# Kernel optimization log

Measured on AMD Instinct MI355X. Metric: run time of the kernel, lower is better.

## Reference

```python
import jax, jax.numpy as jnp
import numpy as np

GRID_SIZE = 8
IN_DIM = 1024
OUT_DIM = 1024
BATCH = 4096


def setup_inputs() -> dict:
    key = jax.random.key(0)
    k1, k2, k3 = jax.random.split(key, 3)
    noise_scale = 0.1
    noise_scale_base = 0.1
    x = jax.random.normal(k1, (BATCH, IN_DIM), dtype=jnp.float32)
    scale_base = (1.0 / np.sqrt(IN_DIM)
                  + (jax.random.normal(k2, (OUT_DIM, IN_DIM), dtype=jnp.float32) * 2 - 1)
                  * noise_scale_base)
    scale_spline = jnp.full((OUT_DIM, IN_DIM), 1.0, dtype=jnp.float32)
    coeff = (jax.random.uniform(k3, (2, OUT_DIM, IN_DIM, GRID_SIZE), dtype=jnp.float32)
             * noise_scale / (np.sqrt(IN_DIM) * np.sqrt(GRID_SIZE)))
    return {"x": x, "scale_base": scale_base, "scale_spline": scale_spline,
            "coeff": coeff}


def reference(x, scale_base, scale_spline, coeff):
    # x: (B, I); scale_base/scale_spline: (O, I); coeff: (2, O, I, G)
    G = coeff.shape[-1]
    k = jnp.arange(1, G + 1, dtype=x.dtype)          # (G,)
    ang = x[:, :, None] * k                           # (B, I, G)
    cos_b = jnp.cos(ang)
    sin_b = jnp.sin(ang)
    # fold scale_spline into coeff: (2, O, I, G)
    w = scale_spline[None, :, :, None] * coeff
    spline = (jnp.einsum('big,oig->bo', cos_b, w[0])
              + jnp.einsum('big,oig->bo', sin_b, w[1]))  # (B, O)
    base = jnp.einsum('bi,oi->bo', jax.nn.silu(x), scale_base)
    return base + spline
```

## Files before the change

### kernel.cpp

```cpp
#include <hip/hip_runtime.h>
#include <hip/hip_bf16.h>
#include <stdint.h>

#define BATCH   4096
#define IN_DIM  1024
#define OUT_DIM 1024
#define GRID_G  8
#define K8      16384
#define KB      1024
#define SPLIT8  4
#define WSCALE  256.0f

typedef __bf16 bf16x8 __attribute__((ext_vector_type(8)));
typedef float  f32x4  __attribute__((ext_vector_type(4)));
typedef int    i32x4  __attribute__((ext_vector_type(4)));
typedef int    i32x8  __attribute__((ext_vector_type(8)));

__device__ inline void store_fp8x8(void* p, const float v[8]) {
    int lo = 0, hi = 0;
    lo = __builtin_amdgcn_cvt_pk_fp8_f32(v[0], v[1], lo, false);
    lo = __builtin_amdgcn_cvt_pk_fp8_f32(v[2], v[3], lo, true);
    hi = __builtin_amdgcn_cvt_pk_fp8_f32(v[4], v[5], hi, false);
    hi = __builtin_amdgcn_cvt_pk_fp8_f32(v[6], v[7], hi, true);
    *(int2*)p = make_int2(lo, hi);
}

__global__ void prep(const float* __restrict__ x, const float* __restrict__ sb,
                     const float* __restrict__ ss, const float* __restrict__ coeff,
                     uint8_t* __restrict__ A8, uint8_t* __restrict__ W8,
                     __bf16* __restrict__ Ab, __bf16* __restrict__ Wb) {
    if (blockIdx.x < 2048) {
        int t  = blockIdx.x * blockDim.x + threadIdx.x;
        int b  = t >> 7;
        int i0 = (t & 127) * 8;
        const float4* xp = (const float4*)(x + (size_t)b * IN_DIM + i0);
        float4 x0 = xp[0], x1 = xp[1];
        float xv[8] = {x0.x, x0.y, x0.z, x0.w, x1.x, x1.y, x1.z, x1.w};

        constexpr float INV2PI = 0.15915494309189535f;
        float c1[8], s1[8], ck[8], sk[8];
        bf16x8 v;
#pragma unroll
        for (int j = 0; j < 8; ++j) {
            float xx  = xv[j];
            float sil = xx / (1.f + __expf(-xx));
            v[j] = (__bf16)sil;
            float rev = xx * INV2PI;
            rev -= floorf(rev);
            s1[j] = __builtin_amdgcn_sinf(rev);
            c1[j] = __builtin_amdgcn_cosf(rev);
            ck[j] = c1[j]; sk[j] = s1[j];
        }
        *(bf16x8*)(Ab + (size_t)b * IN_DIM + i0) = v;

        uint8_t* a8 = A8 + (size_t)b * K8 + i0;
#pragma unroll
        for (int g = 1; g <= GRID_G; ++g) {
            float vc[8], vs[8];
#pragma unroll
            for (int j = 0; j < 8; ++j) {
                vc[j] = ck[j];
                vs[j] = sk[j];
                float cn = ck[j] * c1[j] - sk[j] * s1[j];
                float sn = sk[j] * c1[j] + ck[j] * s1[j];
                ck[j] = cn; sk[j] = sn;
            }
            store_fp8x8(a8 + (size_t)(g - 1) * IN_DIM, vc);
            store_fp8x8(a8 + (size_t)(GRID_G + g - 1) * IN_DIM, vs);
        }
    } else {
        int t  = (blockIdx.x - 2048) * blockDim.x + threadIdx.x;
        int o  = t >> 7;
        int i0 = (t & 127) * 8;
        size_t oi = (size_t)o * IN_DIM + i0;

        float s[8];
        {
            const float4* sp = (const float4*)(ss + oi);
            float4 s0 = sp[0], s1v = sp[1];
            s[0]=s0.x; s[1]=s0.y; s[2]=s0.z; s[3]=s0.w;
            s[4]=s1v.x; s[5]=s1v.y; s[6]=s1v.z; s[7]=s1v.w;
        }
        {
            const float4* bp = (const float4*)(sb + oi);
            float4 b0 = bp[0], b1 = bp[1];
            float bv[8] = {b0.x, b0.y, b0.z, b0.w, b1.x, b1.y, b1.z, b1.w};
            bf16x8 v;
#pragma unroll
            for (int j = 0; j < 8; ++j) v[j] = (__bf16)bv[j];
            *(bf16x8*)(Wb + oi) = v;
        }
        uint8_t* w8 = W8 + (size_t)o * K8 + i0;
#pragma unroll
        for (int p = 0; p < 2; ++p) {
            const float* cp = coeff + ((size_t)p * OUT_DIM * IN_DIM + oi) * GRID_G;
            float c[8][8];
#pragma unroll
            for (int j = 0; j < 8; ++j) {
                const float4* cj = (const float4*)(cp + (size_t)j * GRID_G);
                float4 a0 = cj[0], a1 = cj[1];
                c[j][0]=a0.x; c[j][1]=a0.y; c[j][2]=a0.z; c[j][3]=a0.w;
                c[j][4]=a1.x; c[j][5]=a1.y; c[j][6]=a1.z; c[j][7]=a1.w;
            }
#pragma unroll
            for (int g = 0; g < GRID_G; ++g) {
                float v[8];
#pragma unroll
                for (int j = 0; j < 8; ++j) v[j] = s[j] * c[j][g] * WSCALE;
                store_fp8x8(w8 + (size_t)(p * GRID_G + g) * IN_DIM, v);
            }
        }
    }
}

__global__ __launch_bounds__(256, 4) void gemm_all(const uint8_t* __restrict__ A8,
                                                   const uint8_t* __restrict__ W8,
                                                   const uint8_t* __restrict__ Ab,
                                                   const uint8_t* __restrict__ Wb,
                                                   float* __restrict__ C) {
    __shared__ __align__(16) uint8_t As[16384];
    __shared__ __align__(16) uint8_t Bs[16384];
    const int tid = threadIdx.x;
    const int w   = tid >> 6;
    const int l   = tid & 63;
    const int bn  = blockIdx.x;
    const int bm  = blockIdx.y;
    const int kz  = blockIdx.z;
    const int wm  = w & 1;
    const int wn  = w >> 1;

    f32x4 acc[4][4] = {};

    const int srow   = l >> 3;
    const int schunk = ((l & 7) ^ srow) * 16;
    const int lm = l & 15;
    const int q  = l >> 4;
    float oscale;

    if (kz < SPLIT8) {
        const uint8_t* Ag = A8 + (size_t)(bm * 128 + w * 32 + srow) * K8 + kz * (K8 / SPLIT8) + schunk;
        const uint8_t* Bg = W8 + (size_t)(bn * 128 + w * 32 + srow) * K8 + kz * (K8 / SPLIT8) + schunk;
        const int c0 = (q * 2) << 4, c1 = (q * 2 + 1) << 4;

        for (int ks = 0; ks < (K8 / SPLIT8) / 128; ++ks) {
#pragma unroll
            for (int j = 0; j < 4; ++j) {
                __builtin_amdgcn_global_load_lds(
                    (const uint32_t*)(Ag + (size_t)(j * 8) * K8),
                    (uint32_t*)(As + (w * 32 + j * 8) * 128), 16, 0, 0);
                __builtin_amdgcn_global_load_lds(
                    (const uint32_t*)(Bg + (size_t)(j * 8) * K8),
                    (uint32_t*)(Bs + (w * 32 + j * 8) * 128), 16, 0, 0);
            }
            Ag += 128; Bg += 128;
            __syncthreads();

            i32x8 bf[4];
#pragma unroll
            for (int j = 0; j < 4; ++j) {
                const int row = wn * 64 + j * 16 + lm;
                const int sw  = (row & 7) << 4;
                const uint8_t* rp = Bs + row * 128;
                i32x4 lo = *(const i32x4*)(rp + (c0 ^ sw));
                i32x4 hi = *(const i32x4*)(rp + (c1 ^ sw));
                bf[j] = __builtin_shufflevector(lo, hi, 0, 1, 2, 3, 4, 5, 6, 7);
            }
#pragma unroll
            for (int i = 0; i < 4; ++i) {
                const int row = wm * 64 + i * 16 + lm;
                const int sw  = (row & 7) << 4;
                const uint8_t* rp = As + row * 128;
                i32x4 lo = *(const i32x4*)(rp + (c0 ^ sw));
                i32x4 hi = *(const i32x4*)(rp + (c1 ^ sw));
                i32x8 af = __builtin_shufflevector(lo, hi, 0, 1, 2, 3, 4, 5, 6, 7);
#pragma unroll
                for (int j = 0; j < 4; ++j)
                    acc[i][j] = __builtin_amdgcn_mfma_scale_f32_16x16x128_f8f6f4(
                        af, bf[j], acc[i][j], 0, 0, 0, 0x7f7f7f7f, 0, 0x7f7f7f7f);
            }
            __syncthreads();
        }
        oscale = 1.0f / WSCALE;
    } else {
        const uint8_t* Ag = Ab + (size_t)(bm * 128 + w * 32 + srow) * (KB * 2) + schunk;
        const uint8_t* Bg = Wb + (size_t)(bn * 128 + w * 32 + srow) * (KB * 2) + schunk;

        for (int ks = 0; ks < (KB * 2) / 128; ++ks) {
#pragma unroll
            for (int j = 0; j < 4; ++j) {
                __builtin_amdgcn_global_load_lds(
                    (const uint32_t*)(Ag + (size_t)(j * 8) * (KB * 2)),
                    (uint32_t*)(As + (w * 32 + j * 8) * 128), 16, 0, 0);
                __builtin_amdgcn_global_load_lds(
                    (const uint32_t*)(Bg + (size_t)(j * 8) * (KB * 2)),
                    (uint32_t*)(Bs + (w * 32 + j * 8) * 128), 16, 0, 0);
            }
            Ag += 128; Bg += 128;
            __syncthreads();

#pragma unroll
            for (int h = 0; h < 2; ++h) {
                bf16x8 af[4], bfr[4];
#pragma unroll
                for (int i = 0; i < 4; ++i) {
                    const int row = wm * 64 + i * 16 + lm;
                    af[i] = *(const bf16x8*)(As + row * 128 + ((((h * 4 + q) ^ (row & 7))) << 4));
                }
#pragma unroll
                for (int j = 0; j < 4; ++j) {
                    const int row = wn * 64 + j * 16 + lm;
                    bfr[j] = *(const bf16x8*)(Bs + row * 128 + ((((h * 4 + q) ^ (row & 7))) << 4));
                }
#pragma unroll
                for (int i = 0; i < 4; ++i)
#pragma unroll
                    for (int j = 0; j < 4; ++j)
                        acc[i][j] = __builtin_amdgcn_mfma_f32_16x16x32_bf16(af[i], bfr[j], acc[i][j], 0, 0, 0);
            }
            __syncthreads();
        }
        oscale = 1.0f;
    }

    const int row0 = bm * 128 + wm * 64 + q * 4;
    const int col0 = bn * 128 + wn * 64 + lm;
#pragma unroll
    for (int i = 0; i < 4; ++i)
#pragma unroll
        for (int j = 0; j < 4; ++j)
#pragma unroll
            for (int r = 0; r < 4; ++r)
                unsafeAtomicAdd(&C[(size_t)(row0 + i * 16 + r) * OUT_DIM + col0 + j * 16],
                                acc[i][j][r] * oscale);
}

extern "C" void kernel_launch(void* const* d_in, const int* in_sizes, int n_in,
                              void* d_out, int out_size, void* d_ws, size_t ws_size,
                              hipStream_t stream) {
    const float* x     = (const float*)d_in[0];
    const float* sb    = (const float*)d_in[1];
    const float* ss    = (const float*)d_in[2];
    const float* coeff = (const float*)d_in[3];
    float* out = (float*)d_out;

    uint8_t* A8 = (uint8_t*)d_ws;
    uint8_t* W8 = A8 + (size_t)BATCH * K8;
    __bf16*  Ab = (__bf16*)(W8 + (size_t)OUT_DIM * K8);
    __bf16*  Wb = Ab + (size_t)BATCH * KB;

    hipLaunchKernelGGL(prep, dim3(2048 + 512), dim3(256), 0, stream,
                       x, sb, ss, coeff, A8, W8, Ab, Wb);
    hipMemsetAsync(out, 0, (size_t)BATCH * OUT_DIM * sizeof(float), stream);
    hipLaunchKernelGGL(gemm_all, dim3(OUT_DIM / 128, BATCH / 128, SPLIT8 + 1), dim3(256), 0, stream,
                       A8, W8, (const uint8_t*)Ab, (const uint8_t*)Wb, out);
}
```

Measured before the change: 278.1 us.

## Use 256x256 tiles with double-buffered LDS and merge bf16 base into split-K blocks

The GEMM now uses 1024-thread blocks on 256x256 output tiles with double-buffered LDS, so the next K slice is fetched while the current one is computed. Each split-K block handles its fp8 spline slice and then a quarter of the bf16 base GEMM, which removes the separate base z-slice. The base weights are pre-scaled by WSCALE so one output scale applies to both. This trades fewer blocks (64 per split, 256 total) and 128KB of LDS per block for better reuse and overlap, which may limit occupancy.

Measured after the change: 807.6 us. 190% more time.

```diff
diff --git a/kernel.cpp b/kernel.cpp
--- a/kernel.cpp
+++ b/kernel.cpp
@@ -8,7 +8,7 @@
 #define GRID_G  8
 #define K8      16384
 #define KB      1024
-#define SPLIT8  4
+#define SPLITK  4
 #define WSCALE  256.0f
 
 typedef __bf16 bf16x8 __attribute__((ext_vector_type(8)));
@@ -87,7 +87,7 @@
             float bv[8] = {b0.x, b0.y, b0.z, b0.w, b1.x, b1.y, b1.z, b1.w};
             bf16x8 v;
 #pragma unroll
-            for (int j = 0; j < 8; ++j) v[j] = (__bf16)bv[j];
+            for (int j = 0; j < 8; ++j) v[j] = (__bf16)(bv[j] * WSCALE);
             *(bf16x8*)(Wb + oi) = v;
         }
         uint8_t* w8 = W8 + (size_t)o * K8 + i0;
@@ -113,54 +113,69 @@
     }
 }
 
-__global__ __launch_bounds__(256, 4) void gemm_all(const uint8_t* __restrict__ A8,
-                                                   const uint8_t* __restrict__ W8,
-                                                   const uint8_t* __restrict__ Ab,
-                                                   const uint8_t* __restrict__ Wb,
-                                                   float* __restrict__ C) {
-    __shared__ __align__(16) uint8_t As[16384];
-    __shared__ __align__(16) uint8_t Bs[16384];
+__global__ __launch_bounds__(1024, 4) void gemm_all(const uint8_t* __restrict__ A8,
+                                                    const uint8_t* __restrict__ W8,
+                                                    const uint8_t* __restrict__ Ab,
+                                                    const uint8_t* __restrict__ Wb,
+                                                    float* __restrict__ C) {
+    __shared__ __align__(16) uint8_t As[2][256 * 128];
+    __shared__ __align__(16) uint8_t Bs[2][256 * 128];
     const int tid = threadIdx.x;
     const int w   = tid >> 6;
     const int l   = tid & 63;
     const int bn  = blockIdx.x;
     const int bm  = blockIdx.y;
     const int kz  = blockIdx.z;
-    const int wm  = w & 1;
-    const int wn  = w >> 1;
+    const int wm  = w & 3;
+    const int wn  = w >> 2;
 
     f32x4 acc[4][4] = {};
 
-    const int srow   = l >> 3;
-    const int schunk = ((l & 7) ^ srow) * 16;
-    const int lm = l & 15;
-    const int q  = l >> 4;
-    float oscale;
-
-    if (kz < SPLIT8) {
-        const uint8_t* Ag = A8 + (size_t)(bm * 128 + w * 32 + srow) * K8 + kz * (K8 / SPLIT8) + schunk;
-        const uint8_t* Bg = W8 + (size_t)(bn * 128 + w * 32 + srow) * K8 + kz * (K8 / SPLIT8) + schunk;
-        const int c0 = (q * 2) << 4, c1 = (q * 2 + 1) << 4;
-
-        for (int ks = 0; ks < (K8 / SPLIT8) / 128; ++ks) {
-#pragma unroll
-            for (int j = 0; j < 4; ++j) {
-                __builtin_amdgcn_global_load_lds(
-                    (const uint32_t*)(Ag + (size_t)(j * 8) * K8),
-                    (uint32_t*)(As + (w * 32 + j * 8) * 128), 16, 0, 0);
-                __builtin_amdgcn_global_load_lds(
-                    (const uint32_t*)(Bg + (size_t)(j * 8) * K8),
-                    (uint32_t*)(Bs + (w * 32 + j * 8) * 128), 16, 0, 0);
-            }
-            Ag += 128; Bg += 128;
-            __syncthreads();
-
+    const int r   = tid >> 3;
+    const int sch = ((tid & 7) ^ (r & 7)) * 16;
+    const int lm  = l & 15;
+    const int q   = l >> 4;
+    const int ldso1 = w * 1024;
+    const int ldso2 = 16384 + w * 1024;
+
+    const uint8_t* a0 = A8 + (size_t)(bm * 256 + r) * K8 + kz * (K8 / SPLITK) + sch;
+    const uint8_t* a1 = a0 + (size_t)128 * K8;
+    const uint8_t* b0 = W8 + (size_t)(bn * 256 + r) * K8 + kz * (K8 / SPLITK) + sch;
+    const uint8_t* b1 = b0 + (size_t)128 * K8;
+
+    __builtin_amdgcn_global_load_lds((const uint32_t*)a0, (uint32_t*)(As[0] + ldso1), 16, 0, 0);
+    __builtin_amdgcn_global_load_lds((const uint32_t*)a1, (uint32_t*)(As[0] + ldso2), 16, 0, 0);
+    __builtin_amdgcn_global_load_lds((const uint32_t*)b0, (uint32_t*)(Bs[0] + ldso1), 16, 0, 0);
+    __builtin_amdgcn_global_load_lds((const uint32_t*)b1, (uint32_t*)(Bs[0] + ldso2), 16, 0, 0);
+    a0 += 128; a1 += 128; b0 += 128; b1 += 128;
+    __syncthreads();
+
+    const int c0 = (q * 2) << 4, c1 = (q * 2 + 1) << 4;
+    int cur = 0;
+
+    for (int ks = 0; ks < 36; ++ks) {
+        if (ks < 35) {
+            if (ks == 31) {
+                a0 = Ab + (size_t)(bm * 256 + r) * (KB * 2) + kz * (KB * 2 / SPLITK) + sch;
+                a1 = a0 + (size_t)128 * (KB * 2);
+                b0 = Wb + (size_t)(bn * 256 + r) * (KB * 2) + kz * (KB * 2 / SPLITK) + sch;
+                b1 = b0 + (size_t)128 * (KB * 2);
+            }
+            const int nxt = cur ^ 1;
+            __builtin_amdgcn_global_load_lds((const uint32_t*)a0, (uint32_t*)(As[nxt] + ldso1), 16, 0, 0);
+            __builtin_amdgcn_global_load_lds((const uint32_t*)a1, (uint32_t*)(As[nxt] + ldso2), 16, 0, 0);
+            __builtin_amdgcn_global_load_lds((const uint32_t*)b0, (uint32_t*)(Bs[nxt] + ldso1), 16, 0, 0);
+            __builtin_amdgcn_global_load_lds((const uint32_t*)b1, (uint32_t*)(Bs[nxt] + ldso2), 16, 0, 0);
+            a0 += 128; a1 += 128; b0 += 128; b1 += 128;
+        }
+
+        if (ks < 32) {
             i32x8 bf[4];
 #pragma unroll
             for (int j = 0; j < 4; ++j) {
                 const int row = wn * 64 + j * 16 + lm;
                 const int sw  = (row & 7) << 4;
-                const uint8_t* rp = Bs + row * 128;
+                const uint8_t* rp = Bs[cur] + row * 128;
                 i32x4 lo = *(const i32x4*)(rp + (c0 ^ sw));
                 i32x4 hi = *(const i32x4*)(rp + (c1 ^ sw));
                 bf[j] = __builtin_shufflevector(lo, hi, 0, 1, 2, 3, 4, 5, 6, 7);
@@ -169,7 +184,7 @@
             for (int i = 0; i < 4; ++i) {
                 const int row = wm * 64 + i * 16 + lm;
                 const int sw  = (row & 7) << 4;
-                const uint8_t* rp = As + row * 128;
+                const uint8_t* rp = As[cur] + row * 128;
                 i32x4 lo = *(const i32x4*)(rp + (c0 ^ sw));
                 i32x4 hi = *(const i32x4*)(rp + (c1 ^ sw));
                 i32x8 af = __builtin_shufflevector(lo, hi, 0, 1, 2, 3, 4, 5, 6, 7);
@@ -178,38 +193,19 @@
                     acc[i][j] = __builtin_amdgcn_mfma_scale_f32_16x16x128_f8f6f4(
                         af, bf[j], acc[i][j], 0, 0, 0, 0x7f7f7f7f, 0, 0x7f7f7f7f);
             }
-            __syncthreads();
-        }
-        oscale = 1.0f / WSCALE;
-    } else {
-        const uint8_t* Ag = Ab + (size_t)(bm * 128 + w * 32 + srow) * (KB * 2) + schunk;
-        const uint8_t* Bg = Wb + (size_t)(bn * 128 + w * 32 + srow) * (KB * 2) + schunk;
-
-        for (int ks = 0; ks < (KB * 2) / 128; ++ks) {
-#pragma unroll
-            for (int j = 0; j < 4; ++j) {
-                __builtin_amdgcn_global_load_lds(
-                    (const uint32_t*)(Ag + (size_t)(j * 8) * (KB * 2)),
-                    (uint32_t*)(As + (w * 32 + j * 8) * 128), 16, 0, 0);
-                __builtin_amdgcn_global_load_lds(
-                    (const uint32_t*)(Bg + (size_t)(j * 8) * (KB * 2)),
-                    (uint32_t*)(Bs + (w * 32 + j * 8) * 128), 16, 0, 0);
-            }
-            Ag += 128; Bg += 128;
-            __syncthreads();
-
+        } else {
 #pragma unroll
             for (int h = 0; h < 2; ++h) {
                 bf16x8 af[4], bfr[4];
 #pragma unroll
                 for (int i = 0; i < 4; ++i) {
                     const int row = wm * 64 + i * 16 + lm;
-                    af[i] = *(const bf16x8*)(As + row * 128 + ((((h * 4 + q) ^ (row & 7))) << 4));
+                    af[i] = *(const bf16x8*)(As[cur] + row * 128 + ((((h * 4 + q) ^ (row & 7))) << 4));
                 }
 #pragma unroll
                 for (int j = 0; j < 4; ++j) {
                     const int row = wn * 64 + j * 16 + lm;
-                    bfr[j] = *(const bf16x8*)(Bs + row * 128 + ((((h * 4 + q) ^ (row & 7))) << 4));
+                    bfr[j] = *(const bf16x8*)(Bs[cur] + row * 128 + ((((h * 4 + q) ^ (row & 7))) << 4));
                 }
 #pragma unroll
                 for (int i = 0; i < 4; ++i)
@@ -217,21 +213,22 @@
                     for (int j = 0; j < 4; ++j)
                         acc[i][j] = __builtin_amdgcn_mfma_f32_16x16x32_bf16(af[i], bfr[j], acc[i][j], 0, 0, 0);
             }
-            __syncthreads();
-        }
-        oscale = 1.0f;
+        }
+        __syncthreads();
+        cur ^= 1;
     }
 
-    const int row0 = bm * 128 + wm * 64 + q * 4;
-    const int col0 = bn * 128 + wn * 64 + lm;
+    const float inv = 1.0f / WSCALE;
+    const int row0 = bm * 256 + wm * 64 + q * 4;
+    const int col0 = bn * 256 + wn * 64 + lm;
 #pragma unroll
     for (int i = 0; i < 4; ++i)
 #pragma unroll
         for (int j = 0; j < 4; ++j)
 #pragma unroll
-            for (int r = 0; r < 4; ++r)
-                unsafeAtomicAdd(&C[(size_t)(row0 + i * 16 + r) * OUT_DIM + col0 + j * 16],
-                                acc[i][j][r] * oscale);
+            for (int rr = 0; rr < 4; ++rr)
+                unsafeAtomicAdd(&C[(size_t)(row0 + i * 16 + rr) * OUT_DIM + col0 + j * 16],
+                                acc[i][j][rr] * inv);
 }
 
 extern "C" void kernel_launch(void* const* d_in, const int* in_sizes, int n_in,
@@ -251,6 +248,6 @@
     hipLaunchKernelGGL(prep, dim3(2048 + 512), dim3(256), 0, stream,
                        x, sb, ss, coeff, A8, W8, Ab, Wb);
     hipMemsetAsync(out, 0, (size_t)BATCH * OUT_DIM * sizeof(float), stream);
-    hipLaunchKernelGGL(gemm_all, dim3(OUT_DIM / 128, BATCH / 128, SPLIT8 + 1), dim3(256), 0, stream,
+    hipLaunchKernelGGL(gemm_all, dim3(OUT_DIM / 256, BATCH / 256, SPLITK), dim3(1024), 0, stream,
                        A8, W8, (const uint8_t*)Ab, (const uint8_t*)Wb, out);
 }
```
